# Optimization experiments

Measured on AMD Instinct MI355X. Metric: run time of the kernel, lower is better.

## Reference

```python
import jax, jax.numpy as jnp
import numpy as np

N = 100000   # total atoms in the batch
E = 400000   # directed edges (bonds both directions)
F = 11       # raw atom feature dim (Linear(11, vector_dim))
D = 512      # vector_dim
L = 5        # num_conv_layers
G = 2048     # number of molecules (graphs) in the batch


def setup_inputs() -> dict:
    key = jax.random.key(0)
    k = jax.random.split(key, 6)
    x = jax.random.uniform(k[0], (N, F), dtype=jnp.float32)  # nonneg counts-like features
    edge_index = jax.random.randint(k[1], (2, E), 0, N, dtype=jnp.int32)
    batch = jnp.sort(jax.random.randint(k[2], (N,), 0, G, dtype=jnp.int32))
    exp_W = jax.random.normal(k[3], (F, D), dtype=jnp.float32) * (1.0 / np.sqrt(F))
    exp_b = jnp.zeros((D,), dtype=jnp.float32)
    gcn_W = jax.random.normal(k[4], (L, D, D), dtype=jnp.float32) * (1.0 / np.sqrt(D))
    gcn_b = jnp.zeros((L, D), dtype=jnp.float32)
    return {"x": x, "edge_index": edge_index, "batch": batch,
            "exp_W": exp_W, "exp_b": exp_b, "gcn_W": gcn_W, "gcn_b": gcn_b}


def reference(x, edge_index, batch, exp_W, exp_b, gcn_W, gcn_b):
    # GraphEmbedding.forward (eval mode: dropout = identity)
    src, dst = edge_index[0], edge_index[1]
    h = jnp.log(x + 1.0) @ exp_W + exp_b  # expansion Linear(11, D)  -> [N, D]

    # GCN normalization with improved=True: self-loop weight 2.0
    # deg_i = sum of incoming edge weights (1.0) + 2.0 self-loop
    ones_e = jnp.ones((E,), dtype=h.dtype)
    deg = jax.ops.segment_sum(ones_e, dst, num_segments=N) + 2.0
    dinv = jax.lax.rsqrt(deg)              # deg >= 2, always finite
    enorm = dinv[src] * dinv[dst]          # per-edge norm (weight 1.0)
    self_norm = 2.0 * dinv * dinv          # self-loop norm (weight 2.0)

    for l in range(L):
        xw = h @ gcn_W[l]                                   # [N, D]
        msg = enorm[:, None] * xw[src]                      # gather + scale, [E, D]
        agg = jax.ops.segment_sum(msg, dst, num_segments=N)  # scatter-add
        agg = agg + self_norm[:, None] * xw + gcn_b[l]
        h = h + jax.nn.relu(agg)                            # residual + relu (dropout off)

    # global_add_pool over molecules
    return jax.ops.segment_sum(h, batch, num_segments=G)    # [G, D]
```

## Files before the change

kernel.cpp:

```cpp
#include <hip/hip_runtime.h>
#include <hip/hip_bf16.h>
#include <stdint.h>

typedef __attribute__((ext_vector_type(8))) short bf16x8;
typedef __attribute__((ext_vector_type(4))) float f32x4;
typedef unsigned short ushort_t;
typedef unsigned int uint_t;

__device__ __forceinline__ unsigned short f2bf(float f) {
  unsigned u = __float_as_uint(f);
  u += 0x7fffu + ((u >> 16) & 1u);
  return (unsigned short)(u >> 16);
}
__device__ __forceinline__ float bf2f(unsigned u16) {
  return __uint_as_float(u16 << 16);
}
__device__ __forceinline__ void fma8(float* a, uint4 u, float w) {
  a[0] += w * bf2f(u.x & 0xffffu); a[1] += w * bf2f(u.x >> 16);
  a[2] += w * bf2f(u.y & 0xffffu); a[3] += w * bf2f(u.y >> 16);
  a[4] += w * bf2f(u.z & 0xffffu); a[5] += w * bf2f(u.z >> 16);
  a[6] += w * bf2f(u.w & 0xffffu); a[7] += w * bf2f(u.w >> 16);
}
__device__ __forceinline__ uint4 pack8u(const float* a) {
  uint4 p;
  p.x = (uint_t)f2bf(a[0]) | ((uint_t)f2bf(a[1]) << 16);
  p.y = (uint_t)f2bf(a[2]) | ((uint_t)f2bf(a[3]) << 16);
  p.z = (uint_t)f2bf(a[4]) | ((uint_t)f2bf(a[5]) << 16);
  p.w = (uint_t)f2bf(a[6]) | ((uint_t)f2bf(a[7]) << 16);
  return p;
}

__global__ void k_zero(int* __restrict__ p, int n) {
  int i = blockIdx.x * blockDim.x + threadIdx.x;
  if (i < n) p[i] = 0;
}

__global__ void k_prep_w(const float* __restrict__ W, ushort_t* __restrict__ Wt, int total) {
  int idx = blockIdx.x * blockDim.x + threadIdx.x;
  if (idx >= total) return;
  int j   = idx & 7;
  int col = (idx >> 3) & 127;
  int kg  = (idx >> 10) & 3;
  int kt  = (idx >> 12) & 15;
  int nt  = (idx >> 16) & 3;
  int l   = idx >> 18;
  int k = kt * 32 + kg * 8 + j;
  int n = nt * 128 + col;
  Wt[idx] = f2bf(W[((size_t)(l * 512 + k)) * 512 + n]);
}

__global__ __launch_bounds__(256) void k_expand(const float* __restrict__ x,
                                                const float* __restrict__ eW,
                                                const float* __restrict__ eb,
                                                ushort_t* __restrict__ h, int N) {
  const int wid = (blockIdx.x * 256 + threadIdx.x) >> 6;
  const int nw = (gridDim.x * 256) >> 6;
  const int l = threadIdx.x & 63;

  float wf[11][8];
  float bias[8];
#pragma unroll
  for (int f = 0; f < 11; ++f) {
    float4 a = *(const float4*)&eW[f * 512 + l * 8];
    float4 b = *(const float4*)&eW[f * 512 + l * 8 + 4];
    wf[f][0] = a.x; wf[f][1] = a.y; wf[f][2] = a.z; wf[f][3] = a.w;
    wf[f][4] = b.x; wf[f][5] = b.y; wf[f][6] = b.z; wf[f][7] = b.w;
  }
  {
    float4 a = *(const float4*)&eb[l * 8];
    float4 b = *(const float4*)&eb[l * 8 + 4];
    bias[0] = a.x; bias[1] = a.y; bias[2] = a.z; bias[3] = a.w;
    bias[4] = b.x; bias[5] = b.y; bias[6] = b.z; bias[7] = b.w;
  }

  for (int n = wid; n < N; n += nw) {
    float xv = (l < 11) ? x[(size_t)n * 11 + l] : 0.f;
    float lx = log1pf(xv);
    float acc[8];
#pragma unroll
    for (int j = 0; j < 8; ++j) acc[j] = bias[j];
#pragma unroll
    for (int f = 0; f < 11; ++f) {
      float c = __shfl(lx, f, 64);
#pragma unroll
      for (int j = 0; j < 8; ++j) acc[j] += c * wf[f][j];
    }
    *(uint4*)(h + (size_t)n * 512 + l * 8) = pack8u(acc);
  }
}

__global__ void k_deg(const int* __restrict__ dst, int* __restrict__ deg, int E) {
  int e = blockIdx.x * blockDim.x + threadIdx.x;
  if (e < E) atomicAdd(&deg[dst[e]], 1);
}

__global__ void k_dinv(const int* __restrict__ deg, float* __restrict__ dinv,
                       float* __restrict__ selfn, int N) {
  int n = blockIdx.x * blockDim.x + threadIdx.x;
  if (n >= N) return;
  float d = (float)deg[n] + 2.0f;
  dinv[n] = rsqrtf(d);
  selfn[n] = 2.0f / d;
}

__global__ void k_scan_a(const int* __restrict__ deg, int* __restrict__ off,
                         int* __restrict__ bsum, int N) {
  __shared__ int sd[256];
  int t = threadIdx.x;
  int i0 = blockIdx.x * 1024 + t * 4;
  int d[4];
#pragma unroll
  for (int j = 0; j < 4; ++j) d[j] = (i0 + j < N) ? deg[i0 + j] : 0;
  int ts = d[0] + d[1] + d[2] + d[3];
  sd[t] = ts;
  __syncthreads();
  for (int o = 1; o < 256; o <<= 1) {
    int v = (t >= o) ? sd[t - o] : 0;
    __syncthreads();
    sd[t] += v;
    __syncthreads();
  }
  int incl = sd[t];
  int run = incl - ts;
#pragma unroll
  for (int j = 0; j < 4; ++j) {
    if (i0 + j < N) off[i0 + j] = run;
    run += d[j];
  }
  if (t == 255) bsum[blockIdx.x] = incl;
}

__global__ void k_scan_b(const int* __restrict__ bsum, int* __restrict__ bpre, int nb,
                         int* __restrict__ off, int N, int E) {
  __shared__ int sd[256];
  int t = threadIdx.x;
  int v = (t < nb) ? bsum[t] : 0;
  sd[t] = v;
  __syncthreads();
  for (int o = 1; o < 256; o <<= 1) {
    int u = (t >= o) ? sd[t - o] : 0;
    __syncthreads();
    sd[t] += u;
    __syncthreads();
  }
  if (t < nb) bpre[t] = sd[t] - v;
  if (t == 0) off[N] = E;
}

__global__ void k_scan_c(int* __restrict__ off, const int* __restrict__ bpre, int N) {
  int i = blockIdx.x * blockDim.x + threadIdx.x;
  if (i < N) off[i] += bpre[i >> 10];
}

__global__ void k_fill(const int* __restrict__ src, const int* __restrict__ dst,
                       const int* __restrict__ off, int* __restrict__ cur,
                       int* __restrict__ ssrc, int E) {
  int e = blockIdx.x * blockDim.x + threadIdx.x;
  if (e >= E) return;
  int t = dst[e];
  int p = atomicAdd(&cur[t], 1);
  ssrc[off[t] + p] = src[e];
}

__global__ __launch_bounds__(256) void k_agg2(const ushort_t* __restrict__ h,
                                              ushort_t* __restrict__ s,
                                              const int* __restrict__ off,
                                              const int* __restrict__ ssrc,
                                              const float* __restrict__ dinv,
                                              const float* __restrict__ selfn,
                                              int N, int q, int r) {
  const int b = blockIdx.x;
  const int x = b & 7;
  const int ib = b >> 3;
  const int bpx = gridDim.x >> 3;
  const int wv = threadIdx.x >> 6;
  const int l = threadIdx.x & 63;

  auto swz_lo = [&](int xx) { return xx < r ? xx * (q + 1) : r * (q + 1) + (xx - r) * q; };
  const int node_lo = swz_lo(x) * 32;
  const int node_hi = min(N, swz_lo(x + 1) * 32);
  const int stride = bpx * 4 * 2;

  for (int n0 = node_lo + (ib * 4 + wv) * 2; n0 < node_hi; n0 += stride) {
    const int n1 = n0 + 1;
    const bool v1 = n1 < node_hi;
    int i0 = off[n0], e0 = off[n0 + 1];
    int i1 = v1 ? e0 : 0, e1 = v1 ? off[n1 + 1] : 0;
    float dn0 = dinv[n0], dn1 = v1 ? dinv[n1] : 0.f;
    float a0[8], a1[8];
    {
      uint4 u = *(const uint4*)(h + (size_t)n0 * 512 + l * 8);
      float sn = selfn[n0];
      a0[0] = sn * bf2f(u.x & 0xffffu); a0[1] = sn * bf2f(u.x >> 16);
      a0[2] = sn * bf2f(u.y & 0xffffu); a0[3] = sn * bf2f(u.y >> 16);
      a0[4] = sn * bf2f(u.z & 0xffffu); a0[5] = sn * bf2f(u.z >> 16);
      a0[6] = sn * bf2f(u.w & 0xffffu); a0[7] = sn * bf2f(u.w >> 16);
    }
#pragma unroll
    for (int j = 0; j < 8; ++j) a1[j] = 0.f;
    if (v1) {
      uint4 u = *(const uint4*)(h + (size_t)n1 * 512 + l * 8);
      fma8(a1, u, selfn[n1]);
    }

    const int cj = min(e0 - i0, e1 - i1);
    if (cj > 0) {
      int m0 = ssrc[i0], m1 = ssrc[i1];
      float w0 = dn0 * dinv[m0], w1 = dn1 * dinv[m1];
      uint4 u0 = *(const uint4*)(h + (size_t)m0 * 512 + l * 8);
      uint4 u1 = *(const uint4*)(h + (size_t)m1 * 512 + l * 8);
      for (int k = 1; k < cj; ++k) {
        int m0n = ssrc[i0 + k], m1n = ssrc[i1 + k];
        float w0n = dn0 * dinv[m0n], w1n = dn1 * dinv[m1n];
        uint4 u0n = *(const uint4*)(h + (size_t)m0n * 512 + l * 8);
        uint4 u1n = *(const uint4*)(h + (size_t)m1n * 512 + l * 8);
        fma8(a0, u0, w0);
        fma8(a1, u1, w1);
        u0 = u0n; u1 = u1n; w0 = w0n; w1 = w1n;
      }
      fma8(a0, u0, w0);
      fma8(a1, u1, w1);
      i0 += cj; i1 += cj;
    }
    if (i0 < e0) {
      int m = ssrc[i0];
      float w = dn0 * dinv[m];
      uint4 u = *(const uint4*)(h + (size_t)m * 512 + l * 8);
      for (++i0; i0 < e0; ++i0) {
        int mn = ssrc[i0];
        float wn = dn0 * dinv[mn];
        uint4 un = *(const uint4*)(h + (size_t)mn * 512 + l * 8);
        fma8(a0, u, w);
        u = un; w = wn;
      }
      fma8(a0, u, w);
    }
    if (i1 < e1) {
      int m = ssrc[i1];
      float w = dn1 * dinv[m];
      uint4 u = *(const uint4*)(h + (size_t)m * 512 + l * 8);
      for (++i1; i1 < e1; ++i1) {
        int mn = ssrc[i1];
        float wn = dn1 * dinv[mn];
        uint4 un = *(const uint4*)(h + (size_t)mn * 512 + l * 8);
        fma8(a1, u, w);
        u = un; w = wn;
      }
      fma8(a1, u, w);
    }

    *(uint4*)(s + (size_t)n0 * 512 + l * 8) = pack8u(a0);
    if (v1) *(uint4*)(s + (size_t)n1 * 512 + l * 8) = pack8u(a1);
  }
}

__global__ __launch_bounds__(256) void k_gemm(const ushort_t* __restrict__ s,
                                              const ushort_t* __restrict__ Wt,
                                              const float* __restrict__ gbl,
                                              ushort_t* __restrict__ h, int N) {
  __shared__ alignas(16) ushort_t AB[2][8192];
  const int tid = threadIdx.x;

  const int nwg = gridDim.x * gridDim.y;
  const int orig = blockIdx.y * gridDim.x + blockIdx.x;
  const int q = nwg >> 3, r = nwg & 7;
  const int xcd = orig & 7, pos = orig >> 3;
  const int swz = (xcd < r ? xcd * (q + 1) : r * (q + 1) + (xcd - r) * q) + pos;
  const int nt = swz & 3;
  const int m0 = (swz >> 2) * 128;

  const int wv = tid >> 6, ln = tid & 63;
  const int wrow = wv >> 1, wcol = wv & 1;
  const int l15 = ln & 15, l4 = ln >> 4;

  f32x4 acc[4][4];
#pragma unroll
  for (int i = 0; i < 4; ++i)
#pragma unroll
    for (int j = 0; j < 4; ++j) acc[i][j] = (f32x4){0.f, 0.f, 0.f, 0.f};

  const int arow = tid & 127, akg = tid >> 7;
  const ushort_t* pa = s + (size_t)min(m0 + arow, N - 1) * 512 + akg * 8;
  const ushort_t* wtb = Wt + ((size_t)nt << 16);

  auto stage = [&](int kt, int buf) {
    ushort_t* base = &AB[buf][0];
    const ushort_t* a0 = pa + kt * 32;
    __builtin_amdgcn_global_load_lds(
        (const __attribute__((address_space(1))) uint_t*)a0,
        (__attribute__((address_space(3))) uint_t*)&base[tid * 8], 16, 0, 0);
    __builtin_amdgcn_global_load_lds(
        (const __attribute__((address_space(1))) uint_t*)(a0 + 16),
        (__attribute__((address_space(3))) uint_t*)&base[(256 + tid) * 8], 16, 0, 0);
    const ushort_t* wt = wtb + (kt << 12);
    __builtin_amdgcn_global_load_lds(
        (const __attribute__((address_space(1))) uint_t*)(wt + tid * 8),
        (__attribute__((address_space(3))) uint_t*)&base[4096 + tid * 8], 16, 0, 0);
    __builtin_amdgcn_global_load_lds(
        (const __attribute__((address_space(1))) uint_t*)(wt + (256 + tid) * 8),
        (__attribute__((address_space(3))) uint_t*)&base[4096 + (256 + tid) * 8], 16, 0, 0);
  };

  stage(0, 0);
  stage(1, 1);
  asm volatile("s_waitcnt vmcnt(4)" ::: "memory");
  __builtin_amdgcn_s_barrier();

  for (int kt = 0; kt < 16; ++kt) {
    const int cur = kt & 1;
    bf16x8 a[4], b[4];
#pragma unroll
    for (int i = 0; i < 4; ++i)
      a[i] = *(const bf16x8*)&AB[cur][(l4 * 128 + wrow * 64 + i * 16 + l15) * 8];
#pragma unroll
    for (int j = 0; j < 4; ++j)
      b[j] = *(const bf16x8*)&AB[cur][4096 + (l4 * 128 + wcol * 64 + j * 16 + l15) * 8];
    if (kt < 14) {
      asm volatile("s_waitcnt lgkmcnt(0)" ::: "memory");
      __builtin_amdgcn_s_barrier();
      stage(kt + 2, cur);
    }
    __builtin_amdgcn_s_setprio(1);
#pragma unroll
    for (int i = 0; i < 4; ++i)
#pragma unroll
      for (int j = 0; j < 4; ++j)
        acc[i][j] = __builtin_amdgcn_mfma_f32_16x16x32_bf16(a[i], b[j], acc[i][j], 0, 0, 0);
    __builtin_amdgcn_s_setprio(0);
    if (kt < 14) {
      asm volatile("s_waitcnt vmcnt(4)" ::: "memory");
      __builtin_amdgcn_s_barrier();
    } else if (kt == 14) {
      asm volatile("s_waitcnt vmcnt(0)" ::: "memory");
      __builtin_amdgcn_s_barrier();
    }
  }
  __syncthreads();

  float* cst = (float*)&AB[0][0];
#pragma unroll
  for (int p = 0; p < 4; ++p) {
    const int wrow_sel = p >> 1, ipair = (p & 1) * 2;
    if (wrow == wrow_sel) {
#pragma unroll
      for (int ii = 0; ii < 2; ++ii) {
        int i = ipair + ii;
#pragma unroll
        for (int v = 0; v < 4; ++v) {
          int r32 = ii * 16 + l4 * 4 + v;
#pragma unroll
          for (int j = 0; j < 4; ++j)
            cst[r32 * 128 + wcol * 64 + j * 16 + l15] = acc[i][j][v];
        }
      }
    }
    __syncthreads();
#pragma unroll
    for (int k = 0; k < 2; ++k) {
      int u = k * 256 + tid;
      int row_l = u >> 4, cb = u & 15;
      int grow = m0 + wrow_sel * 64 + ipair * 16 + row_l;
      if (grow < N) {
        float4 c0 = *(const float4*)&cst[row_l * 128 + cb * 8];
        float4 c1 = *(const float4*)&cst[row_l * 128 + cb * 8 + 4];
        float c[8] = {c0.x, c0.y, c0.z, c0.w, c1.x, c1.y, c1.z, c1.w};
        const float* gp = gbl + nt * 128 + cb * 8;
        float4 b0 = *(const float4*)gp;
        float4 b1 = *(const float4*)(gp + 4);
        float bb[8] = {b0.x, b0.y, b0.z, b0.w, b1.x, b1.y, b1.z, b1.w};
        ushort_t* hp = h + (size_t)grow * 512 + nt * 128 + cb * 8;
        uint4 hu = *(const uint4*)hp;
        float hv[8];
        hv[0] = bf2f(hu.x & 0xffffu); hv[1] = bf2f(hu.x >> 16);
        hv[2] = bf2f(hu.y & 0xffffu); hv[3] = bf2f(hu.y >> 16);
        hv[4] = bf2f(hu.z & 0xffffu); hv[5] = bf2f(hu.z >> 16);
        hv[6] = bf2f(hu.w & 0xffffu); hv[7] = bf2f(hu.w >> 16);
#pragma unroll
        for (int j = 0; j < 8; ++j) hv[j] += fmaxf(c[j] + bb[j], 0.f);
        *(uint4*)hp = pack8u(hv);
      }
    }
    __syncthreads();
  }
}

__device__ __forceinline__ int lbound(const int* a, int n, int v) {
  int lo = 0, hi = n;
  while (lo < hi) {
    int m = (lo + hi) >> 1;
    if (a[m] < v) lo = m + 1; else hi = m;
  }
  return lo;
}

__global__ __launch_bounds__(256) void k_pool(const ushort_t* __restrict__ h,
                                              const int* __restrict__ batch,
                                              float* __restrict__ out, int N) {
  __shared__ float red[4 * 512];
  int g = blockIdx.x;
  int t = threadIdx.x;
  int w = t >> 6, l = t & 63;
  int start = lbound(batch, N, g);
  int end = lbound(batch, N, g + 1);
  float acc[8];
#pragma unroll
  for (int j = 0; j < 8; ++j) acc[j] = 0.f;
  for (int n = start + w; n < end; n += 4) {
    uint4 u = *(const uint4*)(h + (size_t)n * 512 + l * 8);
    acc[0] += bf2f(u.x & 0xffffu); acc[1] += bf2f(u.x >> 16);
    acc[2] += bf2f(u.y & 0xffffu); acc[3] += bf2f(u.y >> 16);
    acc[4] += bf2f(u.z & 0xffffu); acc[5] += bf2f(u.z >> 16);
    acc[6] += bf2f(u.w & 0xffffu); acc[7] += bf2f(u.w >> 16);
  }
#pragma unroll
  for (int j = 0; j < 8; ++j) red[w * 512 + l * 8 + j] = acc[j];
  __syncthreads();
  if (t < 128) {
    float4 sv = make_float4(0.f, 0.f, 0.f, 0.f);
#pragma unroll
    for (int ww = 0; ww < 4; ++ww) {
      float4 v = *(const float4*)&red[ww * 512 + t * 4];
      sv.x += v.x; sv.y += v.y; sv.z += v.z; sv.w += v.w;
    }
    *(float4*)&out[(size_t)g * 512 + t * 4] = sv;
  }
}

extern "C" void kernel_launch(void* const* d_in, const int* in_sizes, int n_in,
                              void* d_out, int out_size, void* d_ws, size_t ws_size,
                              hipStream_t stream) {
  const float* x  = (const float*)d_in[0];
  const int* ei   = (const int*)d_in[1];
  const int* batch= (const int*)d_in[2];
  const float* eW = (const float*)d_in[3];
  const float* eb = (const float*)d_in[4];
  const float* gW = (const float*)d_in[5];
  const float* gb = (const float*)d_in[6];
  float* out = (float*)d_out;

  const int N = in_sizes[0] / 11;
  const int E = in_sizes[1] / 2;
  const int G = out_size / 512;
  const int L = in_sizes[5] / (512 * 512);

  const int* src = ei;
  const int* dst = ei + E;

  char* p = (char*)d_ws;
  auto carve = [&](size_t bytes) {
    char* q = p;
    p += (bytes + 255) & ~(size_t)255;
    return q;
  };
  ushort_t* h         = (ushort_t*)carve((size_t)N * 512 * 2);
  ushort_t* s         = (ushort_t*)carve((size_t)N * 512 * 2);
  ushort_t* Wt        = (ushort_t*)carve((size_t)L * 512 * 512 * 2);
  int* deg            = (int*)carve((size_t)N * 4);
  float* dinv         = (float*)carve((size_t)N * 4);
  float* selfn        = (float*)carve((size_t)N * 4);
  int* off            = (int*)carve(((size_t)N + 1) * 4);
  int* cur            = (int*)carve((size_t)N * 4);
  int* ssrc           = (int*)carve((size_t)E * 4);
  int* bsum           = (int*)carve(1024);
  int* bpre           = (int*)carve(1024);

  k_zero<<<(N + 255) / 256, 256, 0, stream>>>(deg, N);
  k_zero<<<(N + 255) / 256, 256, 0, stream>>>(cur, N);

  int totW = L * 512 * 512;
  k_prep_w<<<(totW + 255) / 256, 256, 0, stream>>>(gW, Wt, totW);
  k_expand<<<2048, 256, 0, stream>>>(x, eW, eb, h, N);
  k_deg<<<(E + 255) / 256, 256, 0, stream>>>(dst, deg, E);
  k_dinv<<<(N + 255) / 256, 256, 0, stream>>>(deg, dinv, selfn, N);
  int nb = (N + 1023) / 1024;
  k_scan_a<<<nb, 256, 0, stream>>>(deg, off, bsum, N);
  k_scan_b<<<1, 256, 0, stream>>>(bsum, bpre, nb, off, N, E);
  k_scan_c<<<(N + 255) / 256, 256, 0, stream>>>(off, bpre, N);
  k_fill<<<(E + 255) / 256, 256, 0, stream>>>(src, dst, off, cur, ssrc, E);

  dim3 ggrid(4, (N + 127) / 128);
  const int nwg = 4 * ((N + 127) / 128);
  const int q = nwg >> 3, r = nwg & 7;

  for (int l = 0; l < L; ++l) {
    k_agg2<<<2048, 256, 0, stream>>>(h, s, off, ssrc, dinv, selfn, N, q, r);
    k_gemm<<<ggrid, 256, 0, stream>>>(s, Wt + (size_t)l * 512 * 512,
                                      gb + (size_t)l * 512, h, N);
  }
  k_pool<<<G, 256, 0, stream>>>(h, batch, out, N);
}
```

Baseline: 1.077 ms.

## Load GEMM operands directly from global into registers, dropping LDS staging

Measured after the change: 1.272 ms. +18.1%, slower.

```diff
diff --git a/kernel.cpp b/kernel.cpp
--- a/kernel.cpp
+++ b/kernel.cpp
@@ -258,7 +258,7 @@
                                               const ushort_t* __restrict__ Wt,
                                               const float* __restrict__ gbl,
                                               ushort_t* __restrict__ h, int N) {
-  __shared__ alignas(16) ushort_t AB[2][8192];
+  __shared__ alignas(16) float cst[32 * 128];
   const int tid = threadIdx.x;
 
   const int nwg = gridDim.x * gridDim.y;
@@ -279,65 +279,55 @@
 #pragma unroll
     for (int j = 0; j < 4; ++j) acc[i][j] = (f32x4){0.f, 0.f, 0.f, 0.f};
 
-  const int arow = tid & 127, akg = tid >> 7;
-  const ushort_t* pa = s + (size_t)min(m0 + arow, N - 1) * 512 + akg * 8;
-  const ushort_t* wtb = Wt + ((size_t)nt << 16);
-
-  auto stage = [&](int kt, int buf) {
-    ushort_t* base = &AB[buf][0];
-    const ushort_t* a0 = pa + kt * 32;
-    __builtin_amdgcn_global_load_lds(
-        (const __attribute__((address_space(1))) uint_t*)a0,
-        (__attribute__((address_space(3))) uint_t*)&base[tid * 8], 16, 0, 0);
-    __builtin_amdgcn_global_load_lds(
-        (const __attribute__((address_space(1))) uint_t*)(a0 + 16),
-        (__attribute__((address_space(3))) uint_t*)&base[(256 + tid) * 8], 16, 0, 0);
-    const ushort_t* wt = wtb + (kt << 12);
-    __builtin_amdgcn_global_load_lds(
-        (const __attribute__((address_space(1))) uint_t*)(wt + tid * 8),
-        (__attribute__((address_space(3))) uint_t*)&base[4096 + tid * 8], 16, 0, 0);
-    __builtin_amdgcn_global_load_lds(
-        (const __attribute__((address_space(1))) uint_t*)(wt + (256 + tid) * 8),
-        (__attribute__((address_space(3))) uint_t*)&base[4096 + (256 + tid) * 8], 16, 0, 0);
-  };
-
-  stage(0, 0);
-  stage(1, 1);
-  asm volatile("s_waitcnt vmcnt(4)" ::: "memory");
-  __builtin_amdgcn_s_barrier();
-
-  for (int kt = 0; kt < 16; ++kt) {
-    const int cur = kt & 1;
-    bf16x8 a[4], b[4];
+  const ushort_t* pa[4];
+#pragma unroll
+  for (int i = 0; i < 4; ++i) {
+    int row = min(m0 + wrow * 64 + i * 16 + l15, N - 1);
+    pa[i] = s + (size_t)row * 512 + l4 * 8;
+  }
+  const ushort_t* pb[4];
+#pragma unroll
+  for (int j = 0; j < 4; ++j)
+    pb[j] = Wt + ((size_t)nt << 16) + (l4 * 128 + wcol * 64 + j * 16 + l15) * 8;
+
+  bf16x8 A0[4], A1[4], B0[4], B1[4];
+#pragma unroll
+  for (int i = 0; i < 4; ++i) A0[i] = *(const bf16x8*)(pa[i]);
+#pragma unroll
+  for (int j = 0; j < 4; ++j) B0[j] = *(const bf16x8*)(pb[j]);
+
+#pragma unroll
+  for (int kt = 0; kt < 16; kt += 2) {
+    if (kt + 1 < 16) {
+#pragma unroll
+      for (int i = 0; i < 4; ++i) A1[i] = *(const bf16x8*)(pa[i] + (kt + 1) * 32);
+#pragma unroll
+      for (int j = 0; j < 4; ++j) B1[j] = *(const bf16x8*)(pb[j] + (kt + 1) * 4096);
+    }
+    __builtin_amdgcn_s_setprio(1);
 #pragma unroll
     for (int i = 0; i < 4; ++i)
-      a[i] = *(const bf16x8*)&AB[cur][(l4 * 128 + wrow * 64 + i * 16 + l15) * 8];
-#pragma unroll
-    for (int j = 0; j < 4; ++j)
-      b[j] = *(const bf16x8*)&AB[cur][4096 + (l4 * 128 + wcol * 64 + j * 16 + l15) * 8];
-    if (kt < 14) {
-      asm volatile("s_waitcnt lgkmcnt(0)" ::: "memory");
-      __builtin_amdgcn_s_barrier();
-      stage(kt + 2, cur);
-    }
-    __builtin_amdgcn_s_setprio(1);
-#pragma unroll
-    for (int i = 0; i < 4; ++i)
 #pragma unroll
       for (int j = 0; j < 4; ++j)
-        acc[i][j] = __builtin_amdgcn_mfma_f32_16x16x32_bf16(a[i], b[j], acc[i][j], 0, 0, 0);
+        acc[i][j] = __builtin_amdgcn_mfma_f32_16x16x32_bf16(A0[i], B0[j], acc[i][j], 0, 0, 0);
     __builtin_amdgcn_s_setprio(0);
-    if (kt < 14) {
-      asm volatile("s_waitcnt vmcnt(4)" ::: "memory");
-      __builtin_amdgcn_s_barrier();
-    } else if (kt == 14) {
-      asm volatile("s_waitcnt vmcnt(0)" ::: "memory");
-      __builtin_amdgcn_s_barrier();
-    }
-  }
-  __syncthreads();
-
-  float* cst = (float*)&AB[0][0];
+    if (kt + 2 < 16) {
+#pragma unroll
+      for (int i = 0; i < 4; ++i) A0[i] = *(const bf16x8*)(pa[i] + (kt + 2) * 32);
+#pragma unroll
+      for (int j = 0; j < 4; ++j) B0[j] = *(const bf16x8*)(pb[j] + (kt + 2) * 4096);
+    }
+    if (kt + 1 < 16) {
+      __builtin_amdgcn_s_setprio(1);
+#pragma unroll
+      for (int i = 0; i < 4; ++i)
+#pragma unroll
+        for (int j = 0; j < 4; ++j)
+          acc[i][j] = __builtin_amdgcn_mfma_f32_16x16x32_bf16(A1[i], B1[j], acc[i][j], 0, 0, 0);
+      __builtin_amdgcn_s_setprio(0);
+    }
+  }
+
 #pragma unroll
   for (int p = 0; p < 4; ++p) {
     const int wrow_sel = p >> 1, ipair = (p & 1) * 2;
```
